# Kernel optimization log

Hardware: AMD Instinct MI355X
Metric: run time of the kernel (lower is better)

## Reference

```python
import jax, jax.numpy as jnp
import numpy as np

N_NODES = 500_000
N_EDGES = 8_000_000
FEAT = 10
HID = 32
N_TOOLS = 13
N_PRIM = 8


def setup_inputs() -> dict:
    key = jax.random.key(0)
    ks = jax.random.split(key, 10)
    scale = 0.3
    return {
        "x": jax.random.normal(ks[0], (N_NODES, FEAT), dtype=jnp.float32),
        "edge_index": jax.random.randint(ks[1], (2, N_EDGES), 0, N_NODES, dtype=jnp.int64),
        "w_self": jax.random.normal(ks[2], (FEAT, HID), dtype=jnp.float32) * scale,
        "b_self": jax.random.normal(ks[3], (HID,), dtype=jnp.float32) * scale,
        "w_neigh": jax.random.normal(ks[4], (FEAT, HID), dtype=jnp.float32) * scale,
        "b_neigh": jax.random.normal(ks[5], (HID,), dtype=jnp.float32) * scale,
        "w_act": jax.random.normal(ks[6], (HID, N_TOOLS), dtype=jnp.float32) * scale,
        "b_act": jax.random.normal(ks[7], (N_TOOLS,), dtype=jnp.float32) * scale,
        "w_prim": jax.random.normal(ks[8], (HID, N_PRIM), dtype=jnp.float32) * scale,
        "b_prim": jax.random.normal(ks[9], (N_PRIM,), dtype=jnp.float32) * scale,
    }


def reference(x, edge_index, w_self, b_self, w_neigh, b_neigh, w_act, b_act, w_prim, b_prim):
    n = x.shape[0]
    src, dst = edge_index[0], edge_index[1]
    # mean aggregation over incoming neighbors: scatter-add then count-normalize
    agg = jax.ops.segment_sum(x[src], dst, num_segments=n)            # [N, FEAT]
    count = jax.ops.segment_sum(jnp.ones_like(src, dtype=x.dtype), dst, num_segments=n)
    agg = agg / jnp.maximum(count, 1.0)[:, None]                      # zeros stay zero where count==0
    # dual linear + relu (module applies relu twice; idempotent, apply once)
    h = jax.nn.relu(x @ w_self + b_self + agg @ w_neigh + b_neigh)    # [N, HID]
    graph_embed = jnp.mean(h, axis=0, keepdims=True)                  # [1, HID]
    action_logits = graph_embed @ w_act + b_act                       # [1, N_TOOLS]
    primitive_logits = graph_embed @ w_prim + b_prim                  # [1, N_PRIM]
    return (action_logits, primitive_logits, graph_embed, h)
```

## Files before the change

kernel.cpp:

```cpp
#include <hip/hip_runtime.h>

#define N_NODES 500000
#define N_EDGES 8000000
#define FEAT 10
#define HID 32
#define N_TOOLS 13
#define N_PRIM 8

#define BK_BITS 8
#define BK_SIZE (1 << BK_BITS)
#define NB ((N_NODES + BK_SIZE - 1) / BK_SIZE)
#define SC_THREADS 512
#define SC_EPT 16
#define SC_CHUNK (SC_THREADS * SC_EPT)
#define SC_BLOCKS ((N_EDGES + SC_CHUNK - 1) / SC_CHUNK)
#define R_CH 8
#define ROWS_PER_CH ((SC_BLOCKS + R_CH - 1) / R_CH)

#define LOG_S 2
#define NSLICE (1 << LOG_S)

#define ACC_W 4
#define CELL_W (BK_SIZE * ACC_W)

static __device__ __forceinline__ unsigned q12(float v) {
    int q = (int)floorf(fmaf(v, 256.0f, 2048.5f));
    q = q < 0 ? 0 : (q > 4095 ? 4095 : q);
    return (unsigned)q;
}

static __device__ __forceinline__ int chunk_of_block(int orig) {
    const int q = SC_BLOCKS >> 3, r = SC_BLOCKS & 7;
    const int xcd = orig & 7;
    const int i = orig >> 3;
    const int base = (xcd < r) ? xcd * (q + 1) : r * (q + 1) + (xcd - r) * q;
    return base + i;
}

__global__ __launch_bounds__(SC_THREADS) void bhist_pack_kernel(
    const int* __restrict__ dst, const float* __restrict__ x,
    int* __restrict__ bhist, uint4* __restrict__ xq) {
    __shared__ int hist[NB];
    const int t = threadIdx.x;

    const int node = blockIdx.x * SC_THREADS + t;
    if (node < N_NODES) {
        const float* xr = x + (size_t)node * FEAT;
        unsigned c0 = q12(xr[0]), c1 = q12(xr[1]), c2 = q12(xr[2]);
        unsigned c3 = q12(xr[3]), c4 = q12(xr[4]), c5 = q12(xr[5]);
        unsigned c6 = q12(xr[6]), c7 = q12(xr[7]), c8 = q12(xr[8]);
        unsigned c9 = q12(xr[9]);
        uint4 u;
        u.x = c0 | (c1 << 12) | ((c8 & 0xFF) << 24);
        u.y = c2 | (c3 << 12) | ((c8 >> 8) << 24) | ((c9 >> 8) << 28);
        u.z = c4 | (c5 << 12) | ((c9 & 0xFF) << 24);
        u.w = c6 | (c7 << 12);
        xq[node] = u;
    }

    const int chunk = chunk_of_block(blockIdx.x);
    for (int i = t; i < NB; i += SC_THREADS) hist[i] = 0;
    __syncthreads();
    const int base4 = chunk * (SC_CHUNK / 4);
#pragma unroll
    for (int k = 0; k < SC_EPT / 4; ++k) {
        int i4 = base4 + k * SC_THREADS + t;
        if (i4 * 4 < N_EDGES) {
            int4 d4 = ((const int4*)dst)[i4];
            atomicAdd(&hist[d4.x >> BK_BITS], 1);
            atomicAdd(&hist[d4.y >> BK_BITS], 1);
            atomicAdd(&hist[d4.z >> BK_BITS], 1);
            atomicAdd(&hist[d4.w >> BK_BITS], 1);
        }
    }
    __syncthreads();
    int* row = bhist + (size_t)chunk * NB;
    for (int i = t; i < NB; i += SC_THREADS) row[i] = hist[i];
}

__global__ __launch_bounds__(256) void scan_a_kernel(
    const int* __restrict__ bhist, int* __restrict__ ctmp) {
    const int rc = blockIdx.x >> 3;
    const int cc = blockIdx.x & 7;
    const int c = cc * 256 + threadIdx.x;
    if (c >= NB) return;
    const int r0 = rc * ROWS_PER_CH;
    const int r1 = (r0 + ROWS_PER_CH < SC_BLOCKS) ? r0 + ROWS_PER_CH : SC_BLOCKS;
    int s = 0;
    for (int r = r0; r < r1; ++r) s += bhist[(size_t)r * NB + c];
    ctmp[rc * NB + c] = s;
}

__global__ __launch_bounds__(256) void scan_b_kernel(
    const int* __restrict__ ctmp, int* __restrict__ bstart,
    int* __restrict__ cstart) {
    __shared__ int colt[NB];
    __shared__ int tsum[256];
    const int t = threadIdx.x;
    for (int c = t; c < NB; c += 256) {
        int s = 0;
#pragma unroll
        for (int rc = 0; rc < R_CH; ++rc) s += ctmp[rc * NB + c];
        colt[c] = s;
    }
    __syncthreads();
    const int CPT = (NB + 255) / 256;
    const int c0 = t * CPT;
    int ls = 0;
    for (int k = 0; k < CPT; ++k) {
        int c = c0 + k;
        if (c < NB) ls += colt[c];
    }
    tsum[t] = ls;
    __syncthreads();
    for (int off = 1; off < 256; off <<= 1) {
        int v = (t >= off) ? tsum[t - off] : 0;
        __syncthreads();
        tsum[t] += v;
        __syncthreads();
    }
    int run = tsum[t] - ls;
    for (int k = 0; k < CPT; ++k) {
        int c = c0 + k;
        if (c < NB) {
            int v = colt[c];
            colt[c] = run;
            run += v;
        }
    }
    if (t == 255) bstart[NB] = run;
    __syncthreads();
    for (int c = t; c < NB; c += 256) {
        int r2 = colt[c];
        bstart[c] = r2;
#pragma unroll
        for (int rc = 0; rc < R_CH; ++rc) {
            cstart[rc * NB + c] = r2;
            r2 += ctmp[rc * NB + c];
        }
    }
}

__global__ __launch_bounds__(256) void scan_c_kernel(
    int* __restrict__ bhist, const int* __restrict__ cstart) {
    const int rc = blockIdx.x >> 3;
    const int cc = blockIdx.x & 7;
    const int c = cc * 256 + threadIdx.x;
    if (c >= NB) return;
    const int r0 = rc * ROWS_PER_CH;
    const int r1 = (r0 + ROWS_PER_CH < SC_BLOCKS) ? r0 + ROWS_PER_CH : SC_BLOCKS;
    int run = cstart[rc * NB + c];
    for (int r = r0; r < r1; ++r) {
        size_t i = (size_t)r * NB + c;
        int v = bhist[i];
        bhist[i] = run;
        run += v;
    }
}

__global__ __launch_bounds__(SC_THREADS) void mscatter_kernel(
    const int* __restrict__ src, const int* __restrict__ dst,
    const int* __restrict__ bhist, int* __restrict__ store) {
    __shared__ int lofs[NB];
    __shared__ int tsum[SC_THREADS];
    __shared__ int sstore[SC_CHUNK];
    __shared__ int sbkt[SC_CHUNK];
    const int t = threadIdx.x;
    const int chunk = chunk_of_block(blockIdx.x);
    for (int i = t; i < NB; i += SC_THREADS) lofs[i] = 0;
    __syncthreads();

    const int base = chunk * SC_CHUNK;
    const int nhere = (N_EDGES - base < SC_CHUNK) ? (N_EDGES - base) : SC_CHUNK;
    int bkt[SC_EPT], rnk[SC_EPT], pkd[SC_EPT];
    const int base4 = base >> 2;
#pragma unroll
    for (int k = 0; k < SC_EPT / 4; ++k) {
        const int i4 = base4 + k * SC_THREADS + t;
        const int e0 = k * 4;
        if (i4 * 4 < N_EDGES) {
            int4 d4 = ((const int4*)dst)[i4];
            int4 s4 = ((const int4*)src)[i4];
            bkt[e0 + 0] = d4.x >> BK_BITS;
            pkd[e0 + 0] = ((d4.x & (BK_SIZE - 1)) << 19) | s4.x;
            rnk[e0 + 0] = atomicAdd(&lofs[bkt[e0 + 0]], 1);
            bkt[e0 + 1] = d4.y >> BK_BITS;
            pkd[e0 + 1] = ((d4.y & (BK_SIZE - 1)) << 19) | s4.y;
            rnk[e0 + 1] = atomicAdd(&lofs[bkt[e0 + 1]], 1);
            bkt[e0 + 2] = d4.z >> BK_BITS;
            pkd[e0 + 2] = ((d4.z & (BK_SIZE - 1)) << 19) | s4.z;
            rnk[e0 + 2] = atomicAdd(&lofs[bkt[e0 + 2]], 1);
            bkt[e0 + 3] = d4.w >> BK_BITS;
            pkd[e0 + 3] = ((d4.w & (BK_SIZE - 1)) << 19) | s4.w;
            rnk[e0 + 3] = atomicAdd(&lofs[bkt[e0 + 3]], 1);
        } else {
            bkt[e0 + 0] = bkt[e0 + 1] = bkt[e0 + 2] = bkt[e0 + 3] = -1;
        }
    }
    __syncthreads();

    const int CPT = (NB + SC_THREADS - 1) / SC_THREADS;
    const int c0 = t * CPT;
    int ls = 0;
#pragma unroll
    for (int k = 0; k < CPT; ++k) {
        int c = c0 + k;
        if (c < NB) ls += lofs[c];
    }
    tsum[t] = ls;
    __syncthreads();
    for (int off = 1; off < SC_THREADS; off <<= 1) {
        int v = (t >= off) ? tsum[t - off] : 0;
        __syncthreads();
        tsum[t] += v;
        __syncthreads();
    }
    int run = tsum[t] - ls;
#pragma unroll
    for (int k = 0; k < CPT; ++k) {
        int c = c0 + k;
        if (c < NB) {
            int v = lofs[c];
            lofs[c] = run;
            run += v;
        }
    }
    __syncthreads();

#pragma unroll
    for (int k = 0; k < SC_EPT; ++k) {
        if (bkt[k] >= 0) {
            int p = lofs[bkt[k]] + rnk[k];
            sstore[p] = pkd[k];
            sbkt[p] = bkt[k];
        }
    }
    __syncthreads();

    const int* row = bhist + (size_t)chunk * NB;
#pragma unroll
    for (int k = 0; k < CPT; ++k) {
        int c = c0 + k;
        if (c < NB) lofs[c] = row[c] - lofs[c];
    }
    __syncthreads();

    for (int i = t; i < nhere; i += SC_THREADS) {
        int b = sbkt[i];
        store[lofs[b] + i] = sstore[i];
    }
}

__global__ __launch_bounds__(256) void baggr_a_kernel(
    const int* __restrict__ bstart, const int* __restrict__ store,
    const uint4* __restrict__ xq, unsigned long long* __restrict__ partial) {
    __shared__ unsigned long long lagg64[CELL_W];
    const int t = threadIdx.x;
    const int b = blockIdx.x >> LOG_S;
    const int s = blockIdx.x & (NSLICE - 1);
    for (int i = t; i < CELL_W; i += 256) lagg64[i] = 0ull;
    __syncthreads();

    const int s0 = bstart[b], e0 = bstart[b + 1];
    const int slo = s << (19 - LOG_S);
    const int shi = slo + (1 << (19 - LOG_S));
    for (int o = s0 + t; o < e0; o += 256) {
        int v = store[o];
        int srcn = v & 0x7FFFF;
        if (srcn >= slo && srcn < shi) {
            int loc = v >> 19;
            uint4 u = xq[srcn];
            unsigned long long c0 = u.x & 0xFFF, c1 = (u.x >> 12) & 0xFFF;
            unsigned long long c2 = u.y & 0xFFF, c3 = (u.y >> 12) & 0xFFF;
            unsigned long long c4 = u.z & 0xFFF, c5 = (u.z >> 12) & 0xFFF;
            unsigned long long c6 = u.w & 0xFFF, c7 = (u.w >> 12) & 0xFFF;
            unsigned long long c8 = (u.x >> 24) | (((u.y >> 24) & 0xFu) << 8);
            unsigned long long c9 = (u.z >> 24) | ((u.y >> 28) << 8);
            unsigned long long* la = lagg64 + loc * ACC_W;
            atomicAdd(&la[0], c0 | (c1 << 21) | (c2 << 42));
            atomicAdd(&la[1], c3 | (c4 << 21) | (c5 << 42));
            atomicAdd(&la[2], c6 | (c7 << 21) | (c8 << 42));
            atomicAdd(&la[3], c9 | (1ull << 21));
        }
    }
    __syncthreads();
    unsigned long long* pc = partial + (size_t)blockIdx.x * CELL_W;
    for (int i = t; i < CELL_W; i += 256) pc[i] = lagg64[i];
}

__global__ __launch_bounds__(256) void baggr_b_kernel(
    const unsigned long long* __restrict__ partial,
    const float* __restrict__ x,
    const float* __restrict__ w_self, const float* __restrict__ b_self,
    const float* __restrict__ w_neigh, const float* __restrict__ b_neigh,
    float* __restrict__ h_out, float* __restrict__ hsum) {
    __shared__ unsigned long long lagg64[CELL_W];
    __shared__ float lagg[BK_SIZE * FEAT];
    __shared__ float lcnt[BK_SIZE];
    __shared__ float red[4][HID];
    const int t = threadIdx.x;
    const int b = blockIdx.x;
    const int j = t & 31;
    float ws[FEAT], wn[FEAT];
#pragma unroll
    for (int k = 0; k < FEAT; ++k) {
        ws[k] = w_self[k * HID + j];
        wn[k] = w_neigh[k * HID + j];
    }
    const float bias = b_self[j] + b_neigh[j];

    const unsigned long long* pb = partial + ((size_t)b << LOG_S) * CELL_W;
    for (int i = t; i < CELL_W; i += 256) {
        unsigned long long sv = 0ull;
#pragma unroll
        for (int ss = 0; ss < NSLICE; ++ss) sv += pb[(size_t)ss * CELL_W + i];
        lagg64[i] = sv;
    }
    __syncthreads();

    {
        const unsigned long long w0 = lagg64[t * ACC_W + 0];
        const unsigned long long w1 = lagg64[t * ACC_W + 1];
        const unsigned long long w2 = lagg64[t * ACC_W + 2];
        const unsigned long long w3 = lagg64[t * ACC_W + 3];
        const int cnt = (int)((w3 >> 21) & 0x1FFFFF);
        const float base = -2048.0f * (float)cnt;
        const float sc = 0.00390625f;
        float* la = lagg + t * FEAT;
        la[0] = ((float)(int)(w0 & 0x1FFFFF) + base) * sc;
        la[1] = ((float)(int)((w0 >> 21) & 0x1FFFFF) + base) * sc;
        la[2] = ((float)(int)((w0 >> 42) & 0x1FFFFF) + base) * sc;
        la[3] = ((float)(int)(w1 & 0x1FFFFF) + base) * sc;
        la[4] = ((float)(int)((w1 >> 21) & 0x1FFFFF) + base) * sc;
        la[5] = ((float)(int)((w1 >> 42) & 0x1FFFFF) + base) * sc;
        la[6] = ((float)(int)(w2 & 0x1FFFFF) + base) * sc;
        la[7] = ((float)(int)((w2 >> 21) & 0x1FFFFF) + base) * sc;
        la[8] = ((float)(int)((w2 >> 42) & 0x1FFFFF) + base) * sc;
        la[9] = ((float)(int)(w3 & 0x1FFFFF) + base) * sc;
        lcnt[t] = (float)cnt;
    }
    __syncthreads();

    const int node0 = b << BK_BITS;
    const int lim = (N_NODES - node0 < BK_SIZE) ? (N_NODES - node0) : BK_SIZE;
    float partialh = 0.0f;
#pragma unroll 4
    for (int k = 0; k < 32; ++k) {
        int idx = (k << 8) + t;
        int nl = idx >> 5;
        if (nl < lim) {
            float inv = 1.0f / fmaxf(lcnt[nl], 1.0f);
            const float* xr = x + (size_t)(node0 + nl) * FEAT;
            const float* la = lagg + nl * FEAT;
            float acc = bias;
#pragma unroll
            for (int kk = 0; kk < FEAT; ++kk)
                acc += xr[kk] * ws[kk] + la[kk] * inv * wn[kk];
            acc = fmaxf(acc, 0.0f);
            h_out[(size_t)node0 * HID + idx] = acc;
            partialh += acc;
        }
    }

    partialh += __shfl_down(partialh, 32);
    const int wave = t >> 6, lane = t & 63;
    if (lane < 32) red[wave][lane] = partialh;
    __syncthreads();
    if (t < 32) {
        float s2 = red[0][t] + red[1][t] + red[2][t] + red[3][t];
        atomicAdd(&hsum[t], s2);
    }
}

__global__ __launch_bounds__(256) void baggr_fused_kernel(
    const int* __restrict__ bstart, const int* __restrict__ store,
    const float* __restrict__ x, const uint4* __restrict__ xq,
    const float* __restrict__ w_self, const float* __restrict__ b_self,
    const float* __restrict__ w_neigh, const float* __restrict__ b_neigh,
    float* __restrict__ h_out, float* __restrict__ hsum) {
    __shared__ unsigned long long lagg64[CELL_W];
    __shared__ float lagg[BK_SIZE * FEAT];
    __shared__ float lcnt[BK_SIZE];
    __shared__ float red[4][HID];
    const int t = threadIdx.x;
    const int b = blockIdx.x;
    const int j = t & 31;
    float ws[FEAT], wn[FEAT];
#pragma unroll
    for (int k = 0; k < FEAT; ++k) {
        ws[k] = w_self[k * HID + j];
        wn[k] = w_neigh[k * HID + j];
    }
    const float bias = b_self[j] + b_neigh[j];

    for (int i = t; i < CELL_W; i += 256) lagg64[i] = 0ull;
    __syncthreads();

    const int s0 = bstart[b], e0 = bstart[b + 1];
    for (int o = s0 + t; o < e0; o += 256) {
        int v = store[o];
        int srcn = v & 0x7FFFF;
        int loc = v >> 19;
        uint4 u = xq[srcn];
        unsigned long long c0 = u.x & 0xFFF, c1 = (u.x >> 12) & 0xFFF;
        unsigned long long c2 = u.y & 0xFFF, c3 = (u.y >> 12) & 0xFFF;
        unsigned long long c4 = u.z & 0xFFF, c5 = (u.z >> 12) & 0xFFF;
        unsigned long long c6 = u.w & 0xFFF, c7 = (u.w >> 12) & 0xFFF;
        unsigned long long c8 = (u.x >> 24) | (((u.y >> 24) & 0xFu) << 8);
        unsigned long long c9 = (u.z >> 24) | ((u.y >> 28) << 8);
        unsigned long long* la = lagg64 + loc * ACC_W;
        atomicAdd(&la[0], c0 | (c1 << 21) | (c2 << 42));
        atomicAdd(&la[1], c3 | (c4 << 21) | (c5 << 42));
        atomicAdd(&la[2], c6 | (c7 << 21) | (c8 << 42));
        atomicAdd(&la[3], c9 | (1ull << 21));
    }
    __syncthreads();

    {
        const unsigned long long w0 = lagg64[t * ACC_W + 0];
        const unsigned long long w1 = lagg64[t * ACC_W + 1];
        const unsigned long long w2 = lagg64[t * ACC_W + 2];
        const unsigned long long w3 = lagg64[t * ACC_W + 3];
        const int cnt = (int)((w3 >> 21) & 0x1FFFFF);
        const float base = -2048.0f * (float)cnt;
        const float sc = 0.00390625f;
        float* la = lagg + t * FEAT;
        la[0] = ((float)(int)(w0 & 0x1FFFFF) + base) * sc;
        la[1] = ((float)(int)((w0 >> 21) & 0x1FFFFF) + base) * sc;
        la[2] = ((float)(int)((w0 >> 42) & 0x1FFFFF) + base) * sc;
        la[3] = ((float)(int)(w1 & 0x1FFFFF) + base) * sc;
        la[4] = ((float)(int)((w1 >> 21) & 0x1FFFFF) + base) * sc;
        la[5] = ((float)(int)((w1 >> 42) & 0x1FFFFF) + base) * sc;
        la[6] = ((float)(int)(w2 & 0x1FFFFF) + base) * sc;
        la[7] = ((float)(int)((w2 >> 21) & 0x1FFFFF) + base) * sc;
        la[8] = ((float)(int)((w2 >> 42) & 0x1FFFFF) + base) * sc;
        la[9] = ((float)(int)(w3 & 0x1FFFFF) + base) * sc;
        lcnt[t] = (float)cnt;
    }
    __syncthreads();

    const int node0 = b << BK_BITS;
    const int lim = (N_NODES - node0 < BK_SIZE) ? (N_NODES - node0) : BK_SIZE;
    float partial = 0.0f;
#pragma unroll 4
    for (int k = 0; k < 32; ++k) {
        int idx = (k << 8) + t;
        int nl = idx >> 5;
        if (nl < lim) {
            float inv = 1.0f / fmaxf(lcnt[nl], 1.0f);
            const float* xr = x + (size_t)(node0 + nl) * FEAT;
            const float* la = lagg + nl * FEAT;
            float acc = bias;
#pragma unroll
            for (int kk = 0; kk < FEAT; ++kk)
                acc += xr[kk] * ws[kk] + la[kk] * inv * wn[kk];
            acc = fmaxf(acc, 0.0f);
            h_out[(size_t)node0 * HID + idx] = acc;
            partial += acc;
        }
    }

    partial += __shfl_down(partial, 32);
    const int wave = t >> 6, lane = t & 63;
    if (lane < 32) red[wave][lane] = partial;
    __syncthreads();
    if (t < 32) {
        float s2 = red[0][t] + red[1][t] + red[2][t] + red[3][t];
        atomicAdd(&hsum[t], s2);
    }
}

__global__ void head_kernel(const float* __restrict__ hsum,
                            const float* __restrict__ w_act,
                            const float* __restrict__ b_act,
                            const float* __restrict__ w_prim,
                            const float* __restrict__ b_prim,
                            float* __restrict__ out) {
    __shared__ float ge[HID];
    const int t = threadIdx.x;
    if (t < HID) {
        const float g = hsum[t] * (1.0f / (float)N_NODES);
        ge[t] = g;
        out[N_TOOLS + N_PRIM + t] = g;
    }
    __syncthreads();
    if (t < N_TOOLS) {
        float a = b_act[t];
#pragma unroll
        for (int jj = 0; jj < HID; ++jj) a += ge[jj] * w_act[jj * N_TOOLS + t];
        out[t] = a;
    }
    if (t >= 32 && t < 32 + N_PRIM) {
        const int p = t - 32;
        float a = b_prim[p];
#pragma unroll
        for (int jj = 0; jj < HID; ++jj) a += ge[jj] * w_prim[jj * N_PRIM + p];
        out[N_TOOLS + p] = a;
    }
}

__global__ void scatter_kernel(const int* __restrict__ src,
                               const int* __restrict__ dst,
                               const float* __restrict__ x,
                               float* __restrict__ agg,
                               float* __restrict__ cnt) {
    int e = blockIdx.x * blockDim.x + threadIdx.x;
    if (e >= N_EDGES) return;
    int s = src[e];
    int d = dst[e];
    const float* xr = x + (size_t)s * FEAT;
    float* ar = agg + (size_t)d * FEAT;
#pragma unroll
    for (int k = 0; k < FEAT; ++k) atomicAdd(&ar[k], xr[k]);
    atomicAdd(&cnt[d], 1.0f);
}

__global__ void node_kernel(const float* __restrict__ x,
                            const float* __restrict__ agg,
                            const float* __restrict__ cnt,
                            const float* __restrict__ w_self,
                            const float* __restrict__ b_self,
                            const float* __restrict__ w_neigh,
                            const float* __restrict__ b_neigh,
                            float* __restrict__ h_out,
                            float* __restrict__ hsum) {
    const int j = threadIdx.x & 31;
    float ws[FEAT], wn[FEAT];
#pragma unroll
    for (int k = 0; k < FEAT; ++k) {
        ws[k] = w_self[k * HID + j];
        wn[k] = w_neigh[k * HID + j];
    }
    const float bias = b_self[j] + b_neigh[j];
    const long total = (long)N_NODES * HID;
    const long stride = (long)gridDim.x * blockDim.x;
    float partial = 0.0f;
    for (long idx = (long)blockIdx.x * blockDim.x + threadIdx.x; idx < total;
         idx += stride) {
        const int i = (int)(idx >> 5);
        const float inv = 1.0f / fmaxf(cnt[i], 1.0f);
        const float* xr = x + (size_t)i * FEAT;
        const float* ar = agg + (size_t)i * FEAT;
        float acc = bias;
#pragma unroll
        for (int k = 0; k < FEAT; ++k) {
            acc += xr[k] * ws[k];
            acc += (ar[k] * inv) * wn[k];
        }
        acc = fmaxf(acc, 0.0f);
        h_out[idx] = acc;
        partial += acc;
    }
    partial += __shfl_down(partial, 32);
    __shared__ float red[4][HID];
    const int wave = threadIdx.x >> 6;
    const int lane = threadIdx.x & 63;
    if (lane < 32) red[wave][lane] = partial;
    __syncthreads();
    if (threadIdx.x < 32) {
        float s = red[0][threadIdx.x] + red[1][threadIdx.x] +
                  red[2][threadIdx.x] + red[3][threadIdx.x];
        atomicAdd(&hsum[threadIdx.x], s);
    }
}

extern "C" void kernel_launch(void* const* d_in, const int* in_sizes, int n_in,
                              void* d_out, int out_size, void* d_ws,
                              size_t ws_size, hipStream_t stream) {
    const float* x       = (const float*)d_in[0];
    const int*   ei      = (const int*)d_in[1];
    const float* w_self  = (const float*)d_in[2];
    const float* b_self  = (const float*)d_in[3];
    const float* w_neigh = (const float*)d_in[4];
    const float* b_neigh = (const float*)d_in[5];
    const float* w_act   = (const float*)d_in[6];
    const float* b_act   = (const float*)d_in[7];
    const float* w_prim  = (const float*)d_in[8];
    const float* b_prim  = (const float*)d_in[9];
    float* out = (float*)d_out;
    const int* src = ei;
    const int* dst = ei + N_EDGES;

    const size_t n_bhist = (size_t)SC_BLOCKS * NB;
    const size_t n_ctmp  = (size_t)R_CH * NB;
    const size_t n_bst   = NB + 1;
    const size_t base_elems =
        n_bhist + 2 * n_ctmp + n_bst + (size_t)N_EDGES + HID;
    const size_t xq_ofs  = (base_elems + 3) & ~(size_t)3;
    const size_t n_xq    = (size_t)N_NODES * 4;
    const size_t p_ofs   = xq_ofs + n_xq;
    const size_t n_part  = (size_t)NB * NSLICE * CELL_W * 2;
    const size_t need_fused = (xq_ofs + n_xq) * 4;
    const size_t need_full  = (p_ofs + n_part) * 4;

    if (ws_size >= need_fused) {
        int*   bhist  = (int*)d_ws;
        int*   ctmp   = bhist + n_bhist;
        int*   cstart = ctmp + n_ctmp;
        int*   bstart = cstart + n_ctmp;
        int*   store  = bstart + n_bst;
        float* hsum   = (float*)(store + N_EDGES);
        uint4* xq     = (uint4*)((int*)d_ws + xq_ofs);
        unsigned long long* partial =
            (unsigned long long*)((int*)d_ws + p_ofs);

        hipMemsetAsync(hsum, 0, HID * sizeof(float), stream);

        bhist_pack_kernel<<<SC_BLOCKS, SC_THREADS, 0, stream>>>(dst, x, bhist,
                                                                xq);
        scan_a_kernel<<<64, 256, 0, stream>>>(bhist, ctmp);
        scan_b_kernel<<<1, 256, 0, stream>>>(ctmp, bstart, cstart);
        scan_c_kernel<<<64, 256, 0, stream>>>(bhist, cstart);
        mscatter_kernel<<<SC_BLOCKS, SC_THREADS, 0, stream>>>(src, dst, bhist,
                                                              store);
        if (ws_size >= need_full) {
            baggr_a_kernel<<<NB * NSLICE, 256, 0, stream>>>(bstart, store, xq,
                                                            partial);
            baggr_b_kernel<<<NB, 256, 0, stream>>>(
                partial, x, w_self, b_self, w_neigh, b_neigh,
                out + (N_TOOLS + N_PRIM + HID), hsum);
        } else {
            baggr_fused_kernel<<<NB, 256, 0, stream>>>(
                bstart, store, x, xq, w_self, b_self, w_neigh, b_neigh,
                out + (N_TOOLS + N_PRIM + HID), hsum);
        }
        head_kernel<<<1, 64, 0, stream>>>(hsum, w_act, b_act, w_prim, b_prim,
                                          out);
    } else {
        float* agg  = (float*)d_ws;
        float* cnt  = agg + (size_t)N_NODES * FEAT;
        float* hsum = cnt + N_NODES;
        const size_t zero_bytes =
            ((size_t)N_NODES * FEAT + N_NODES + HID) * sizeof(float);
        hipMemsetAsync(d_ws, 0, zero_bytes, stream);

        scatter_kernel<<<(N_EDGES + 255) / 256, 256, 0, stream>>>(src, dst, x,
                                                                  agg, cnt);
        node_kernel<<<4096, 256, 0, stream>>>(
            x, agg, cnt, w_self, b_self, w_neigh, b_neigh,
            out + (N_TOOLS + N_PRIM + HID), hsum);
        head_kernel<<<1, 64, 0, stream>>>(hsum, w_act, b_act, w_prim, b_prim,
                                          out);
    }
}
```

Before: 359.7 us.

## Reuse histogram ranks in scatter and stage node features in LDS

The histogram kernel now stores each edge's within-chunk rank as a 16-bit value, so the scatter kernel no longer repeats the shared-memory atomics. It instead loads the per-chunk counts and the separately stored bucket offsets (scan_c now writes to a new boffs array rather than overwriting bhist). The scatter's bucket staging array shrinks to 16-bit. The baggr_b kernel also stages x rows and the aggregates into padded LDS rows for vectorized reads. These trade extra global traffic (a rank array of N_EDGES u16, writes and reads of boffs) for fewer LDS atomics and better-coalesced loads.

```diff
diff --git a/kernel.cpp b/kernel.cpp
--- a/kernel.cpp
+++ b/kernel.cpp
@@ -23,6 +23,8 @@
 #define ACC_W 4
 #define CELL_W (BK_SIZE * ACC_W)
 
+#define PADF 12
+
 static __device__ __forceinline__ unsigned q12(float v) {
     int q = (int)floorf(fmaf(v, 256.0f, 2048.5f));
     q = q < 0 ? 0 : (q > 4095 ? 4095 : q);
@@ -39,7 +41,8 @@
 
 __global__ __launch_bounds__(SC_THREADS) void bhist_pack_kernel(
     const int* __restrict__ dst, const float* __restrict__ x,
-    int* __restrict__ bhist, uint4* __restrict__ xq) {
+    int* __restrict__ bhist, unsigned short* __restrict__ rnk16,
+    uint4* __restrict__ xq) {
     __shared__ int hist[NB];
     const int t = threadIdx.x;
 
@@ -67,10 +70,12 @@
         int i4 = base4 + k * SC_THREADS + t;
         if (i4 * 4 < N_EDGES) {
             int4 d4 = ((const int4*)dst)[i4];
-            atomicAdd(&hist[d4.x >> BK_BITS], 1);
-            atomicAdd(&hist[d4.y >> BK_BITS], 1);
-            atomicAdd(&hist[d4.z >> BK_BITS], 1);
-            atomicAdd(&hist[d4.w >> BK_BITS], 1);
+            ushort4 r;
+            r.x = (unsigned short)atomicAdd(&hist[d4.x >> BK_BITS], 1);
+            r.y = (unsigned short)atomicAdd(&hist[d4.y >> BK_BITS], 1);
+            r.z = (unsigned short)atomicAdd(&hist[d4.z >> BK_BITS], 1);
+            r.w = (unsigned short)atomicAdd(&hist[d4.w >> BK_BITS], 1);
+            ((ushort4*)rnk16)[i4] = r;
         }
     }
     __syncthreads();
@@ -142,7 +147,8 @@
 }
 
 __global__ __launch_bounds__(256) void scan_c_kernel(
-    int* __restrict__ bhist, const int* __restrict__ cstart) {
+    const int* __restrict__ bhist, const int* __restrict__ cstart,
+    int* __restrict__ boffs) {
     const int rc = blockIdx.x >> 3;
     const int cc = blockIdx.x & 7;
     const int c = cc * 256 + threadIdx.x;
@@ -152,51 +158,27 @@
     int run = cstart[rc * NB + c];
     for (int r = r0; r < r1; ++r) {
         size_t i = (size_t)r * NB + c;
-        int v = bhist[i];
-        bhist[i] = run;
-        run += v;
+        boffs[i] = run;
+        run += bhist[i];
     }
 }
 
 __global__ __launch_bounds__(SC_THREADS) void mscatter_kernel(
     const int* __restrict__ src, const int* __restrict__ dst,
-    const int* __restrict__ bhist, int* __restrict__ store) {
+    const unsigned short* __restrict__ rnk16,
+    const int* __restrict__ bhist, const int* __restrict__ boffs,
+    int* __restrict__ store) {
     __shared__ int lofs[NB];
     __shared__ int tsum[SC_THREADS];
     __shared__ int sstore[SC_CHUNK];
-    __shared__ int sbkt[SC_CHUNK];
+    __shared__ unsigned short sbkt[SC_CHUNK];
     const int t = threadIdx.x;
     const int chunk = chunk_of_block(blockIdx.x);
-    for (int i = t; i < NB; i += SC_THREADS) lofs[i] = 0;
-    __syncthreads();
-
     const int base = chunk * SC_CHUNK;
     const int nhere = (N_EDGES - base < SC_CHUNK) ? (N_EDGES - base) : SC_CHUNK;
-    int bkt[SC_EPT], rnk[SC_EPT], pkd[SC_EPT];
-    const int base4 = base >> 2;
-#pragma unroll
-    for (int k = 0; k < SC_EPT / 4; ++k) {
-        const int i4 = base4 + k * SC_THREADS + t;
-        const int e0 = k * 4;
-        if (i4 * 4 < N_EDGES) {
-            int4 d4 = ((const int4*)dst)[i4];
-            int4 s4 = ((const int4*)src)[i4];
-            bkt[e0 + 0] = d4.x >> BK_BITS;
-            pkd[e0 + 0] = ((d4.x & (BK_SIZE - 1)) << 19) | s4.x;
-            rnk[e0 + 0] = atomicAdd(&lofs[bkt[e0 + 0]], 1);
-            bkt[e0 + 1] = d4.y >> BK_BITS;
-            pkd[e0 + 1] = ((d4.y & (BK_SIZE - 1)) << 19) | s4.y;
-            rnk[e0 + 1] = atomicAdd(&lofs[bkt[e0 + 1]], 1);
-            bkt[e0 + 2] = d4.z >> BK_BITS;
-            pkd[e0 + 2] = ((d4.z & (BK_SIZE - 1)) << 19) | s4.z;
-            rnk[e0 + 2] = atomicAdd(&lofs[bkt[e0 + 2]], 1);
-            bkt[e0 + 3] = d4.w >> BK_BITS;
-            pkd[e0 + 3] = ((d4.w & (BK_SIZE - 1)) << 19) | s4.w;
-            rnk[e0 + 3] = atomicAdd(&lofs[bkt[e0 + 3]], 1);
-        } else {
-            bkt[e0 + 0] = bkt[e0 + 1] = bkt[e0 + 2] = bkt[e0 + 3] = -1;
-        }
-    }
+
+    const int* crow = bhist + (size_t)chunk * NB;
+    for (int i = t; i < NB; i += SC_THREADS) lofs[i] = crow[i];
     __syncthreads();
 
     const int CPT = (NB + SC_THREADS - 1) / SC_THREADS;
@@ -227,27 +209,40 @@
     }
     __syncthreads();
 
-#pragma unroll
-    for (int k = 0; k < SC_EPT; ++k) {
-        if (bkt[k] >= 0) {
-            int p = lofs[bkt[k]] + rnk[k];
-            sstore[p] = pkd[k];
-            sbkt[p] = bkt[k];
-        }
-    }
-    __syncthreads();
-
-    const int* row = bhist + (size_t)chunk * NB;
+    const int base4 = base >> 2;
+#pragma unroll
+    for (int k = 0; k < SC_EPT / 4; ++k) {
+        int i4 = base4 + k * SC_THREADS + t;
+        if (i4 * 4 < N_EDGES) {
+            int4 d4 = ((const int4*)dst)[i4];
+            int4 s4 = ((const int4*)src)[i4];
+            ushort4 r4 = ((const ushort4*)rnk16)[i4];
+            int b0 = d4.x >> BK_BITS, p0 = lofs[b0] + r4.x;
+            sstore[p0] = ((d4.x & (BK_SIZE - 1)) << 19) | s4.x;
+            sbkt[p0] = (unsigned short)b0;
+            int b1 = d4.y >> BK_BITS, p1 = lofs[b1] + r4.y;
+            sstore[p1] = ((d4.y & (BK_SIZE - 1)) << 19) | s4.y;
+            sbkt[p1] = (unsigned short)b1;
+            int b2 = d4.z >> BK_BITS, p2 = lofs[b2] + r4.z;
+            sstore[p2] = ((d4.z & (BK_SIZE - 1)) << 19) | s4.z;
+            sbkt[p2] = (unsigned short)b2;
+            int b3 = d4.w >> BK_BITS, p3 = lofs[b3] + r4.w;
+            sstore[p3] = ((d4.w & (BK_SIZE - 1)) << 19) | s4.w;
+            sbkt[p3] = (unsigned short)b3;
+        }
+    }
+    __syncthreads();
+
+    const int* orow = boffs + (size_t)chunk * NB;
 #pragma unroll
     for (int k = 0; k < CPT; ++k) {
         int c = c0 + k;
-        if (c < NB) lofs[c] = row[c] - lofs[c];
+        if (c < NB) lofs[c] = orow[c] - lofs[c];
     }
     __syncthreads();
 
     for (int i = t; i < nhere; i += SC_THREADS) {
-        int b = sbkt[i];
-        store[lofs[b] + i] = sstore[i];
+        store[lofs[sbkt[i]] + i] = sstore[i];
     }
 }
 
@@ -295,6 +290,109 @@
     const float* __restrict__ w_neigh, const float* __restrict__ b_neigh,
     float* __restrict__ h_out, float* __restrict__ hsum) {
     __shared__ unsigned long long lagg64[CELL_W];
+    __shared__ float lagg[BK_SIZE * PADF];
+    __shared__ float xs[BK_SIZE * PADF];
+    __shared__ float lcnt[BK_SIZE];
+    __shared__ float red[4][HID];
+    const int t = threadIdx.x;
+    const int b = blockIdx.x;
+    const int j = t & 31;
+    float ws[FEAT], wn[FEAT];
+#pragma unroll
+    for (int k = 0; k < FEAT; ++k) {
+        ws[k] = w_self[k * HID + j];
+        wn[k] = w_neigh[k * HID + j];
+    }
+    const float bias = b_self[j] + b_neigh[j];
+
+    const int node0 = b << BK_BITS;
+    const int lim = (N_NODES - node0 < BK_SIZE) ? (N_NODES - node0) : BK_SIZE;
+
+    const float* xsrc = x + (size_t)node0 * FEAT;
+    const int nfl = lim * FEAT;
+    for (int i = t; i < nfl; i += 256) {
+        int nl = i / FEAT;
+        int kk = i - nl * FEAT;
+        xs[nl * PADF + kk] = xsrc[i];
+    }
+
+    const unsigned long long* pb = partial + ((size_t)b << LOG_S) * CELL_W;
+    for (int i = t; i < CELL_W; i += 256) {
+        unsigned long long sv = 0ull;
+#pragma unroll
+        for (int ss = 0; ss < NSLICE; ++ss) sv += pb[(size_t)ss * CELL_W + i];
+        lagg64[i] = sv;
+    }
+    __syncthreads();
+
+    {
+        const unsigned long long w0 = lagg64[t * ACC_W + 0];
+        const unsigned long long w1 = lagg64[t * ACC_W + 1];
+        const unsigned long long w2 = lagg64[t * ACC_W + 2];
+        const unsigned long long w3 = lagg64[t * ACC_W + 3];
+        const int cnt = (int)((w3 >> 21) & 0x1FFFFF);
+        const float base = -2048.0f * (float)cnt;
+        const float sc = 0.00390625f;
+        float* la = lagg + t * PADF;
+        la[0] = ((float)(int)(w0 & 0x1FFFFF) + base) * sc;
+        la[1] = ((float)(int)((w0 >> 21) & 0x1FFFFF) + base) * sc;
+        la[2] = ((float)(int)((w0 >> 42) & 0x1FFFFF) + base) * sc;
+        la[3] = ((float)(int)(w1 & 0x1FFFFF) + base) * sc;
+        la[4] = ((float)(int)((w1 >> 21) & 0x1FFFFF) + base) * sc;
+        la[5] = ((float)(int)((w1 >> 42) & 0x1FFFFF) + base) * sc;
+        la[6] = ((float)(int)(w2 & 0x1FFFFF) + base) * sc;
+        la[7] = ((float)(int)((w2 >> 21) & 0x1FFFFF) + base) * sc;
+        la[8] = ((float)(int)((w2 >> 42) & 0x1FFFFF) + base) * sc;
+        la[9] = ((float)(int)(w3 & 0x1FFFFF) + base) * sc;
+        lcnt[t] = (float)cnt;
+    }
+    __syncthreads();
+
+    float partialh = 0.0f;
+#pragma unroll 4
+    for (int k = 0; k < 32; ++k) {
+        int idx = (k << 8) + t;
+        int nl = idx >> 5;
+        if (nl < lim) {
+            float inv = 1.0f / fmaxf(lcnt[nl], 1.0f);
+            const float4* xv = (const float4*)(xs + nl * PADF);
+            const float4* av = (const float4*)(lagg + nl * PADF);
+            float4 x0 = xv[0], x1 = xv[1];
+            float2 x2 = *(const float2*)(xs + nl * PADF + 8);
+            float4 a0 = av[0], a1 = av[1];
+            float2 a2 = *(const float2*)(lagg + nl * PADF + 8);
+            float acc = bias;
+            acc += x0.x * ws[0] + x0.y * ws[1] + x0.z * ws[2] + x0.w * ws[3];
+            acc += x1.x * ws[4] + x1.y * ws[5] + x1.z * ws[6] + x1.w * ws[7];
+            acc += x2.x * ws[8] + x2.y * ws[9];
+            float accn = a0.x * wn[0] + a0.y * wn[1] + a0.z * wn[2] +
+                         a0.w * wn[3];
+            accn += a1.x * wn[4] + a1.y * wn[5] + a1.z * wn[6] + a1.w * wn[7];
+            accn += a2.x * wn[8] + a2.y * wn[9];
+            acc += accn * inv;
+            acc = fmaxf(acc, 0.0f);
+            h_out[(size_t)node0 * HID + idx] = acc;
+            partialh += acc;
+        }
+    }
+
+    partialh += __shfl_down(partialh, 32);
+    const int wave = t >> 6, lane = t & 63;
+    if (lane < 32) red[wave][lane] = partialh;
+    __syncthreads();
+    if (t < 32) {
+        float s2 = red[0][t] + red[1][t] + red[2][t] + red[3][t];
+        atomicAdd(&hsum[t], s2);
+    }
+}
+
+__global__ __launch_bounds__(256) void baggr_fused_kernel(
+    const int* __restrict__ bstart, const int* __restrict__ store,
+    const float* __restrict__ x, const uint4* __restrict__ xq,
+    const float* __restrict__ w_self, const float* __restrict__ b_self,
+    const float* __restrict__ w_neigh, const float* __restrict__ b_neigh,
+    float* __restrict__ h_out, float* __restrict__ hsum) {
+    __shared__ unsigned long long lagg64[CELL_W];
     __shared__ float lagg[BK_SIZE * FEAT];
     __shared__ float lcnt[BK_SIZE];
     __shared__ float red[4][HID];
@@ -309,12 +407,26 @@
     }
     const float bias = b_self[j] + b_neigh[j];
 
-    const unsigned long long* pb = partial + ((size_t)b << LOG_S) * CELL_W;
-    for (int i = t; i < CELL_W; i += 256) {
-        unsigned long long sv = 0ull;
-#pragma unroll
-        for (int ss = 0; ss < NSLICE; ++ss) sv += pb[(size_t)ss * CELL_W + i];
-        lagg64[i] = sv;
+    for (int i = t; i < CELL_W; i += 256) lagg64[i] = 0ull;
+    __syncthreads();
+
+    const int s0 = bstart[b], e0 = bstart[b + 1];
+    for (int o = s0 + t; o < e0; o += 256) {
+        int v = store[o];
+        int srcn = v & 0x7FFFF;
+        int loc = v >> 19;
+        uint4 u = xq[srcn];
+        unsigned long long c0 = u.x & 0xFFF, c1 = (u.x >> 12) & 0xFFF;
+        unsigned long long c2 = u.y & 0xFFF, c3 = (u.y >> 12) & 0xFFF;
+        unsigned long long c4 = u.z & 0xFFF, c5 = (u.z >> 12) & 0xFFF;
+        unsigned long long c6 = u.w & 0xFFF, c7 = (u.w >> 12) & 0xFFF;
+        unsigned long long c8 = (u.x >> 24) | (((u.y >> 24) & 0xFu) << 8);
+        unsigned long long c9 = (u.z >> 24) | ((u.y >> 28) << 8);
+        unsigned long long* la = lagg64 + loc * ACC_W;
+        atomicAdd(&la[0], c0 | (c1 << 21) | (c2 << 42));
+        atomicAdd(&la[1], c3 | (c4 << 21) | (c5 << 42));
+        atomicAdd(&la[2], c6 | (c7 << 21) | (c8 << 42));
+        atomicAdd(&la[3], c9 | (1ull << 21));
     }
     __syncthreads();
 
@@ -343,104 +455,6 @@
 
     const int node0 = b << BK_BITS;
     const int lim = (N_NODES - node0 < BK_SIZE) ? (N_NODES - node0) : BK_SIZE;
-    float partialh = 0.0f;
-#pragma unroll 4
-    for (int k = 0; k < 32; ++k) {
-        int idx = (k << 8) + t;
-        int nl = idx >> 5;
-        if (nl < lim) {
-            float inv = 1.0f / fmaxf(lcnt[nl], 1.0f);
-            const float* xr = x + (size_t)(node0 + nl) * FEAT;
-            const float* la = lagg + nl * FEAT;
-            float acc = bias;
-#pragma unroll
-            for (int kk = 0; kk < FEAT; ++kk)
-                acc += xr[kk] * ws[kk] + la[kk] * inv * wn[kk];
-            acc = fmaxf(acc, 0.0f);
-            h_out[(size_t)node0 * HID + idx] = acc;
-            partialh += acc;
-        }
-    }
-
-    partialh += __shfl_down(partialh, 32);
-    const int wave = t >> 6, lane = t & 63;
-    if (lane < 32) red[wave][lane] = partialh;
-    __syncthreads();
-    if (t < 32) {
-        float s2 = red[0][t] + red[1][t] + red[2][t] + red[3][t];
-        atomicAdd(&hsum[t], s2);
-    }
-}
-
-__global__ __launch_bounds__(256) void baggr_fused_kernel(
-    const int* __restrict__ bstart, const int* __restrict__ store,
-    const float* __restrict__ x, const uint4* __restrict__ xq,
-    const float* __restrict__ w_self, const float* __restrict__ b_self,
-    const float* __restrict__ w_neigh, const float* __restrict__ b_neigh,
-    float* __restrict__ h_out, float* __restrict__ hsum) {
-    __shared__ unsigned long long lagg64[CELL_W];
-    __shared__ float lagg[BK_SIZE * FEAT];
-    __shared__ float lcnt[BK_SIZE];
-    __shared__ float red[4][HID];
-    const int t = threadIdx.x;
-    const int b = blockIdx.x;
-    const int j = t & 31;
-    float ws[FEAT], wn[FEAT];
-#pragma unroll
-    for (int k = 0; k < FEAT; ++k) {
-        ws[k] = w_self[k * HID + j];
-        wn[k] = w_neigh[k * HID + j];
-    }
-    const float bias = b_self[j] + b_neigh[j];
-
-    for (int i = t; i < CELL_W; i += 256) lagg64[i] = 0ull;
-    __syncthreads();
-
-    const int s0 = bstart[b], e0 = bstart[b + 1];
-    for (int o = s0 + t; o < e0; o += 256) {
-        int v = store[o];
-        int srcn = v & 0x7FFFF;
-        int loc = v >> 19;
-        uint4 u = xq[srcn];
-        unsigned long long c0 = u.x & 0xFFF, c1 = (u.x >> 12) & 0xFFF;
-        unsigned long long c2 = u.y & 0xFFF, c3 = (u.y >> 12) & 0xFFF;
-        unsigned long long c4 = u.z & 0xFFF, c5 = (u.z >> 12) & 0xFFF;
-        unsigned long long c6 = u.w & 0xFFF, c7 = (u.w >> 12) & 0xFFF;
-        unsigned long long c8 = (u.x >> 24) | (((u.y >> 24) & 0xFu) << 8);
-        unsigned long long c9 = (u.z >> 24) | ((u.y >> 28) << 8);
-        unsigned long long* la = lagg64 + loc * ACC_W;
-        atomicAdd(&la[0], c0 | (c1 << 21) | (c2 << 42));
-        atomicAdd(&la[1], c3 | (c4 << 21) | (c5 << 42));
-        atomicAdd(&la[2], c6 | (c7 << 21) | (c8 << 42));
-        atomicAdd(&la[3], c9 | (1ull << 21));
-    }
-    __syncthreads();
-
-    {
-        const unsigned long long w0 = lagg64[t * ACC_W + 0];
-        const unsigned long long w1 = lagg64[t * ACC_W + 1];
-        const unsigned long long w2 = lagg64[t * ACC_W + 2];
-        const unsigned long long w3 = lagg64[t * ACC_W + 3];
-        const int cnt = (int)((w3 >> 21) & 0x1FFFFF);
-        const float base = -2048.0f * (float)cnt;
-        const float sc = 0.00390625f;
-        float* la = lagg + t * FEAT;
-        la[0] = ((float)(int)(w0 & 0x1FFFFF) + base) * sc;
-        la[1] = ((float)(int)((w0 >> 21) & 0x1FFFFF) + base) * sc;
-        la[2] = ((float)(int)((w0 >> 42) & 0x1FFFFF) + base) * sc;
-        la[3] = ((float)(int)(w1 & 0x1FFFFF) + base) * sc;
-        la[4] = ((float)(int)((w1 >> 21) & 0x1FFFFF) + base) * sc;
-        la[5] = ((float)(int)((w1 >> 42) & 0x1FFFFF) + base) * sc;
-        la[6] = ((float)(int)(w2 & 0x1FFFFF) + base) * sc;
-        la[7] = ((float)(int)((w2 >> 21) & 0x1FFFFF) + base) * sc;
-        la[8] = ((float)(int)((w2 >> 42) & 0x1FFFFF) + base) * sc;
-        la[9] = ((float)(int)(w3 & 0x1FFFFF) + base) * sc;
-        lcnt[t] = (float)cnt;
-    }
-    __syncthreads();
-
-    const int node0 = b << BK_BITS;
-    const int lim = (N_NODES - node0 < BK_SIZE) ? (N_NODES - node0) : BK_SIZE;
     float partial = 0.0f;
 #pragma unroll 4
     for (int k = 0; k < 32; ++k) {
@@ -584,35 +598,47 @@
     const size_t n_bhist = (size_t)SC_BLOCKS * NB;
     const size_t n_ctmp  = (size_t)R_CH * NB;
     const size_t n_bst   = NB + 1;
-    const size_t base_elems =
-        n_bhist + 2 * n_ctmp + n_bst + (size_t)N_EDGES + HID;
-    const size_t xq_ofs  = (base_elems + 3) & ~(size_t)3;
-    const size_t n_xq    = (size_t)N_NODES * 4;
-    const size_t p_ofs   = xq_ofs + n_xq;
-    const size_t n_part  = (size_t)NB * NSLICE * CELL_W * 2;
-    const size_t need_fused = (xq_ofs + n_xq) * 4;
-    const size_t need_full  = (p_ofs + n_part) * 4;
+
+    size_t o = 0;
+    const size_t bhist_o  = o; o += n_bhist;
+    const size_t boffs_o  = o; o += n_bhist;
+    const size_t ctmp_o   = o; o += n_ctmp;
+    const size_t cstart_o = o; o += n_ctmp;
+    const size_t bstart_o = o; o += n_bst;
+    o = (o + 3) & ~(size_t)3;
+    const size_t store_o  = o; o += (size_t)N_EDGES;
+    o = (o + 1) & ~(size_t)1;
+    const size_t rnk_o    = o; o += (size_t)N_EDGES / 2;
+    const size_t hsum_o   = o; o += HID;
+    o = (o + 3) & ~(size_t)3;
+    const size_t xq_o     = o; o += (size_t)N_NODES * 4;
+    const size_t part_o   = o;
+    o += (size_t)NB * NSLICE * CELL_W * 2;
+    const size_t need_fused = part_o * 4;
+    const size_t need_full  = o * 4;
 
     if (ws_size >= need_fused) {
-        int*   bhist  = (int*)d_ws;
-        int*   ctmp   = bhist + n_bhist;
-        int*   cstart = ctmp + n_ctmp;
-        int*   bstart = cstart + n_ctmp;
-        int*   store  = bstart + n_bst;
-        float* hsum   = (float*)(store + N_EDGES);
-        uint4* xq     = (uint4*)((int*)d_ws + xq_ofs);
-        unsigned long long* partial =
-            (unsigned long long*)((int*)d_ws + p_ofs);
+        int* wsI = (int*)d_ws;
+        int*   bhist  = wsI + bhist_o;
+        int*   boffs  = wsI + boffs_o;
+        int*   ctmp   = wsI + ctmp_o;
+        int*   cstart = wsI + cstart_o;
+        int*   bstart = wsI + bstart_o;
+        int*   store  = wsI + store_o;
+        unsigned short* rnk16 = (unsigned short*)(wsI + rnk_o);
+        float* hsum   = (float*)(wsI + hsum_o);
+        uint4* xq     = (uint4*)(wsI + xq_o);
+        unsigned long long* partial = (unsigned long long*)(wsI + part_o);
 
         hipMemsetAsync(hsum, 0, HID * sizeof(float), stream);
 
-        bhist_pack_kernel<<<SC_BLOCKS, SC_THREADS, 0, stream>>>(dst, x, bhist,
-                                                                xq);
+        bhist_pack_kernel<<<SC_BLOCKS, SC_THREADS, 0, stream>>>(
+            dst, x, bhist, rnk16, xq);
         scan_a_kernel<<<64, 256, 0, stream>>>(bhist, ctmp);
         scan_b_kernel<<<1, 256, 0, stream>>>(ctmp, bstart, cstart);
-        scan_c_kernel<<<64, 256, 0, stream>>>(bhist, cstart);
-        mscatter_kernel<<<SC_BLOCKS, SC_THREADS, 0, stream>>>(src, dst, bhist,
-                                                              store);
+        scan_c_kernel<<<64, 256, 0, stream>>>(bhist, cstart, boffs);
+        mscatter_kernel<<<SC_BLOCKS, SC_THREADS, 0, stream>>>(
+            src, dst, rnk16, bhist, boffs, store);
         if (ws_size >= need_full) {
             baggr_a_kernel<<<NB * NSLICE, 256, 0, stream>>>(bstart, store, xq,
                                                             partial);
```

Measured after the change: 339.4 us. -5.6%, faster.
